# Kernel tuning notes

Hardware: AMD Instinct MI355X
Metric: run time of the kernel (lower is better)

The kernel has to match this reference:

```python
import jax, jax.numpy as jnp
import numpy as np

M, L, O, D, B = 512, 16, 32, 64, 16
GAMMA = 1.0 / (2.0 * D)  # RBF bandwidth ~ median sq-dist of randn data


def _rbf(X, Y):
    """Gaussian RBF kernel. X:[M,D]; Y:[M2,D] -> [M,M2] or Y:[B,L,D] -> [B,M,L]."""
    x2 = jnp.sum(X * X, axis=-1)
    y2 = jnp.sum(Y * Y, axis=-1)
    if Y.ndim == 3:
        d2 = x2[None, :, None] + y2[:, None, :] - 2.0 * jnp.einsum('md,bld->bml', X, Y)
    else:
        d2 = x2[:, None] + y2[None, :] - 2.0 * X @ Y.T
    return jnp.exp(-GAMMA * d2)


def setup_inputs() -> dict:
    key = jax.random.key(0)
    k1, k2, k3, k4 = jax.random.split(key, 4)
    inps = jax.random.normal(k1, (B, L, D), dtype=jnp.float32)
    nys_X = jax.random.normal(k2, (M, D), dtype=jnp.float32)
    nys_Y = jax.random.normal(k3, (M, D), dtype=jnp.float32)
    # xavier_uniform for (M*L, M*L)
    lim = float(np.sqrt(6.0 / (2 * M * L)))
    koopman = jax.random.uniform(k4, (M * L, M * L), dtype=jnp.float32, minval=-lim, maxval=lim)
    return {"inps": inps, "nys_X": nys_X, "nys_Y": nys_Y, "koopman": koopman}


def reference(inps, nys_X, nys_Y, koopman):
    scale = M ** (-0.5)
    KX = _rbf(nys_X, inps) * scale   # [B, M, L]
    KY = _rbf(nys_Y, nys_Y) * scale  # [M, M]
    out0 = KX.reshape(B, M * L)      # [B, M*L]

    def step(carry, _):
        nxt = carry @ koopman.T      # einsum('ij,bj->bi', G, out)
        return nxt, nxt

    _, outs = jax.lax.scan(step, out0, None, length=O)   # [O, B, M*L]
    outs = jnp.transpose(outs, (1, 2, 0)).reshape(B, M, L, O)
    outs = jnp.einsum('ij,bjlo->bilo', KY, outs)          # [B, M, L, O]
    outs = jnp.einsum('ja,bjlo->bloa', nys_Y, outs)       # [B, L, O, D]
    return outs
```

## Files before the change

kernel.cpp:

```cpp
#include <hip/hip_runtime.h>
#include <hip/hip_bf16.h>

#define M_  512
#define L_  16
#define O_  32
#define D_  64
#define B_  16
#define ML  8192
#define SLOT (B_*ML)

typedef __attribute__((ext_vector_type(8))) short short8;
typedef __attribute__((ext_vector_type(4))) float f32x4;

static constexpr float GAMMA = 1.0f / 128.0f;
static constexpr float SCALE = 0.0441941738241592f;

__device__ __forceinline__ float sqdiff4(const float4& x, const float4& y) {
    float dx = x.x - y.x, dy = x.y - y.y, dz = x.z - y.z, dw = x.w - y.w;
    return dx*dx + dy*dy + dz*dz + dw*dw;
}

__device__ __forceinline__ unsigned short f2bf(float x) {
    unsigned u = __float_as_uint(x);
    u = (u + 0x7FFFu + ((u >> 16) & 1u)) >> 16;
    return (unsigned short)u;
}

__global__ __launch_bounds__(256) void k_cast(const float* __restrict__ G,
                                              unsigned short* __restrict__ Gb) {
    size_t t = (size_t)blockIdx.x * 256 + threadIdx.x;
    const float4* p = (const float4*)(G + t * 8);
    float4 a = p[0], b = p[1];
    union { short8 v; unsigned short u[8]; } o;
    o.u[0] = f2bf(a.x); o.u[1] = f2bf(a.y); o.u[2] = f2bf(a.z); o.u[3] = f2bf(a.w);
    o.u[4] = f2bf(b.x); o.u[5] = f2bf(b.y); o.u[6] = f2bf(b.z); o.u[7] = f2bf(b.w);
    *(short8*)(Gb + t * 8) = o.v;
}

__global__ __launch_bounds__(256) void k_out0_dual(const float* __restrict__ inps,
                                                   const float* __restrict__ X,
                                                   float* __restrict__ S0,
                                                   unsigned short* __restrict__ C0) {
    int idx = blockIdx.x * 256 + threadIdx.x;
    int l = idx & (L_ - 1);
    int m = (idx >> 4) & (M_ - 1);
    int b = idx >> 13;
    const float* xr = X + m * D_;
    const float* yr = inps + (b * L_ + l) * D_;
    float d2 = 0.f;
#pragma unroll
    for (int d = 0; d < D_; d += 4) {
        float4 xv = *(const float4*)(xr + d);
        float4 yv = *(const float4*)(yr + d);
        d2 += sqdiff4(xv, yv);
    }
    float v = SCALE * expf(-GAMMA * d2);
    S0[idx] = v;
    C0[idx] = f2bf(v);
}

__global__ __launch_bounds__(256) void k_out0(const float* __restrict__ inps,
                                              const float* __restrict__ X,
                                              float* __restrict__ out0) {
    int idx = blockIdx.x * 256 + threadIdx.x;
    int l = idx & (L_ - 1);
    int m = (idx >> 4) & (M_ - 1);
    int b = idx >> 13;
    const float* xr = X + m * D_;
    const float* yr = inps + (b * L_ + l) * D_;
    float d2 = 0.f;
#pragma unroll
    for (int d = 0; d < D_; d += 4) {
        float4 xv = *(const float4*)(xr + d);
        float4 yv = *(const float4*)(yr + d);
        d2 += sqdiff4(xv, yv);
    }
    out0[idx] = SCALE * expf(-GAMMA * d2);
}

__global__ __launch_bounds__(256) void k_ky(const float* __restrict__ Y,
                                            float* __restrict__ KY) {
    int idx = blockIdx.x * 256 + threadIdx.x;
    int j = idx & (M_ - 1);
    int i = idx >> 9;
    const float* yi = Y + i * D_;
    const float* yj = Y + j * D_;
    float d2 = 0.f;
#pragma unroll
    for (int d = 0; d < D_; d += 4) {
        float4 a = *(const float4*)(yi + d);
        float4 b = *(const float4*)(yj + d);
        d2 += sqdiff4(a, b);
    }
    KY[idx] = SCALE * expf(-GAMMA * d2);
}

__global__ __launch_bounds__(256) void k_w(const float* __restrict__ KY,
                                           const float* __restrict__ Y,
                                           float* __restrict__ W) {
    int idx = blockIdx.x * 256 + threadIdx.x;
    int a = idx & (D_ - 1);
    int m = idx >> 6;
    float acc = 0.f;
    for (int j = 0; j < M_; ++j)
        acc = fmaf(KY[m * M_ + j], Y[j * D_ + a], acc);
    W[idx] = acc;
}

__global__ __launch_bounds__(512) void k_step_fused(const unsigned short* __restrict__ Gb,
                                                    const unsigned short* __restrict__ Cin,
                                                    float* __restrict__ Sout,
                                                    unsigned short* __restrict__ Cout) {
    const int i0   = blockIdx.x << 5;
    const int w    = threadIdx.x >> 6;
    const int lane = threadIdx.x & 63;
    const int r    = lane & 15;
    const int koff = (lane >> 4) << 3;
    const size_t kbase = (size_t)w * 1024 + koff;

    const unsigned short* a0 = Gb + (size_t)(i0 + r)      * ML + kbase;
    const unsigned short* a1 = Gb + (size_t)(i0 + 16 + r) * ML + kbase;
    const unsigned short* bp = Cin + (size_t)r * ML + kbase;

    f32x4 acc0 = {0.f, 0.f, 0.f, 0.f};
    f32x4 acc1 = {0.f, 0.f, 0.f, 0.f};
#pragma unroll 4
    for (int k = 0; k < 1024; k += 32) {
        short8 bv = *(const short8*)(bp + k);
        short8 av0 = *(const short8*)(a0 + k);
        short8 av1 = *(const short8*)(a1 + k);
        acc0 = __builtin_amdgcn_mfma_f32_16x16x32_bf16(av0, bv, acc0, 0, 0, 0);
        acc1 = __builtin_amdgcn_mfma_f32_16x16x32_bf16(av1, bv, acc1, 0, 0, 0);
    }

    __shared__ float red[8][512];
    const int rbase = (lane >> 4) << 2;
#pragma unroll
    for (int q = 0; q < 4; ++q) {
        red[w][(rbase + q) * 16 + r]       = acc0[q];
        red[w][256 + (rbase + q) * 16 + r] = acc1[q];
    }
    __syncthreads();

    const int tid = threadIdx.x;
    float s = red[0][tid] + red[1][tid] + red[2][tid] + red[3][tid] +
              red[4][tid] + red[5][tid] + red[6][tid] + red[7][tid];
    const int b = tid & 15;
    const int i = i0 + (tid >> 4);
    Sout[(size_t)b * ML + i] = s;
    Cout[(size_t)b * ML + i] = f2bf(s);
}

__global__ __launch_bounds__(256) void k_step(const float* __restrict__ G,
                                              const float* __restrict__ carry,
                                              float* __restrict__ out) {
    const int i = blockIdx.x;
    const float* __restrict__ grow = G + (size_t)i * ML;
    float acc[B_];
#pragma unroll
    for (int b = 0; b < B_; ++b) acc[b] = 0.f;
    for (int j0 = threadIdx.x * 4; j0 < ML; j0 += 256 * 4) {
        float4 g = *(const float4*)(grow + j0);
#pragma unroll
        for (int b = 0; b < B_; ++b) {
            float4 c = *(const float4*)(carry + b * ML + j0);
            acc[b] = fmaf(g.x, c.x, fmaf(g.y, c.y, fmaf(g.z, c.z, fmaf(g.w, c.w, acc[b]))));
        }
    }
#pragma unroll
    for (int b = 0; b < B_; ++b) {
        float v = acc[b];
#pragma unroll
        for (int off = 32; off > 0; off >>= 1) v += __shfl_down(v, off, 64);
        acc[b] = v;
    }
    __shared__ float red2[4][B_];
    int lane = threadIdx.x & 63;
    int wv   = threadIdx.x >> 6;
    if (lane == 0) {
#pragma unroll
        for (int b = 0; b < B_; ++b) red2[wv][b] = acc[b];
    }
    __syncthreads();
    if (threadIdx.x < B_) {
        float v = red2[0][threadIdx.x] + red2[1][threadIdx.x] +
                  red2[2][threadIdx.x] + red2[3][threadIdx.x];
        out[threadIdx.x * ML + i] = v;
    }
}

__global__ __launch_bounds__(256) void k_final(const float* __restrict__ S,
                                               const float* __restrict__ W,
                                               float* __restrict__ out) {
    int t = blockIdx.x * 256 + threadIdx.x;
    int a = t & (D_ - 1);
    int w = t >> 6;
    int o = w & (O_ - 1);
    int bl = w >> 5;
    int l = bl & (L_ - 1);
    int b = bl >> 4;
    const float* slot = S + (size_t)(o + 1) * SLOT + b * ML;
    float acc = 0.f;
    for (int m = 0; m < M_; ++m)
        acc = fmaf(slot[m * L_ + l], W[m * D_ + a], acc);
    out[t] = acc;
}

extern "C" void kernel_launch(void* const* d_in, const int* in_sizes, int n_in,
                              void* d_out, int out_size, void* d_ws, size_t ws_size,
                              hipStream_t stream) {
    const float* inps    = (const float*)d_in[0];
    const float* nys_X   = (const float*)d_in[1];
    const float* nys_Y   = (const float*)d_in[2];
    const float* koopman = (const float*)d_in[3];
    float* out = (float*)d_out;

    const size_t GB_BYTES  = (size_t)ML * ML * 2;
    const size_t S_BYTES   = (size_t)33 * SLOT * 4;
    const size_t CB_BYTES  = (size_t)33 * SLOT * 2;
    const size_t KY_BYTES  = (size_t)M_ * M_ * 4;
    const size_t W_BYTES   = (size_t)M_ * D_ * 4;
    const size_t NEED_FAST = GB_BYTES + S_BYTES + CB_BYTES + KY_BYTES + W_BYTES;

    if (ws_size >= NEED_FAST) {
        unsigned short* Gb = (unsigned short*)d_ws;
        float*          S  = (float*)((char*)d_ws + GB_BYTES);
        unsigned short* Cb = (unsigned short*)((char*)S + S_BYTES);
        float*          KY = (float*)((char*)Cb + CB_BYTES);
        float*          W  = KY + M_ * M_;

        k_cast<<<(int)((size_t)ML * ML / 8 / 256), 256, 0, stream>>>(koopman, Gb);
        k_out0_dual<<<SLOT / 256, 256, 0, stream>>>(inps, nys_X, S, Cb);
        k_ky<<<(M_ * M_) / 256, 256, 0, stream>>>(nys_Y, KY);
        k_w<<<(M_ * D_) / 256, 256, 0, stream>>>(KY, nys_Y, W);

        for (int o = 1; o <= O_; ++o) {
            k_step_fused<<<256, 512, 0, stream>>>(Gb,
                                                  Cb + (size_t)(o - 1) * SLOT,
                                                  S + (size_t)o * SLOT,
                                                  Cb + (size_t)o * SLOT);
        }
        k_final<<<(B_ * L_ * O_ * D_) / 256, 256, 0, stream>>>(S, W, out);
    } else {
        float* S  = (float*)d_ws;
        float* KY = S + (size_t)33 * SLOT;
        float* W  = KY + M_ * M_;

        k_out0<<<SLOT / 256, 256, 0, stream>>>(inps, nys_X, S);
        k_ky<<<(M_ * M_) / 256, 256, 0, stream>>>(nys_Y, KY);
        k_w<<<(M_ * D_) / 256, 256, 0, stream>>>(KY, nys_Y, W);
        for (int o = 1; o <= O_; ++o)
            k_step<<<ML, 256, 0, stream>>>(koopman, S + (size_t)(o - 1) * SLOT,
                                           S + (size_t)o * SLOT);
        k_final<<<(B_ * L_ * O_ * D_) / 256, 256, 0, stream>>>(S, W, out);
    }
}
```

Before: 958.7 us.

## Pre-pack Koopman matrix into MFMA fragment order and split rows over more blocks

The bf16 cast kernel now writes the Koopman matrix in a tile-packed layout, so each wave's A-fragment loads are fully contiguous 1 KB chunks instead of strided row reads. The step kernel now launches 512 blocks of 1024 threads, one 16-row tile per block, with 16 waves each reducing a 512-wide K slice through shared memory. This raises parallelism and coalescing for the bandwidth-bound 32 GEMV-like steps. In exchange the shared-memory reduction is larger, only a quarter of the threads take part in it, and the B fragment is now loaded once per A tile rather than reused across two tiles.

```diff
diff --git a/kernel.cpp b/kernel.cpp
--- a/kernel.cpp
+++ b/kernel.cpp
@@ -26,15 +26,21 @@
     return (unsigned short)u;
 }
 
-__global__ __launch_bounds__(256) void k_cast(const float* __restrict__ G,
-                                              unsigned short* __restrict__ Gb) {
-    size_t t = (size_t)blockIdx.x * 256 + threadIdx.x;
-    const float4* p = (const float4*)(G + t * 8);
-    float4 a = p[0], b = p[1];
+__global__ __launch_bounds__(256) void k_cast_pack(const float* __restrict__ G,
+                                                   unsigned short* __restrict__ Gp) {
+    int wid  = (blockIdx.x << 2) + (threadIdx.x >> 6);
+    int l    = threadIdx.x & 63;
+    int mt = wid >> 8;
+    int ks = wid & 255;
+    int r  = l & 15;
+    int kk = l >> 4;
+    const float* src = G + (size_t)(mt * 16 + r) * ML + ks * 32 + kk * 8;
+    float4 a = *(const float4*)(src);
+    float4 b = *(const float4*)(src + 4);
     union { short8 v; unsigned short u[8]; } o;
     o.u[0] = f2bf(a.x); o.u[1] = f2bf(a.y); o.u[2] = f2bf(a.z); o.u[3] = f2bf(a.w);
     o.u[4] = f2bf(b.x); o.u[5] = f2bf(b.y); o.u[6] = f2bf(b.z); o.u[7] = f2bf(b.w);
-    *(short8*)(Gb + t * 8) = o.v;
+    *(short8*)(Gp + ((size_t)(mt * 256 + ks) * 64 + l) * 8) = o.v;
 }
 
 __global__ __launch_bounds__(256) void k_out0_dual(const float* __restrict__ inps,
@@ -107,48 +113,44 @@
     W[idx] = acc;
 }
 
-__global__ __launch_bounds__(512) void k_step_fused(const unsigned short* __restrict__ Gb,
-                                                    const unsigned short* __restrict__ Cin,
-                                                    float* __restrict__ Sout,
-                                                    unsigned short* __restrict__ Cout) {
-    const int i0   = blockIdx.x << 5;
+__global__ __launch_bounds__(1024, 8) void k_step_packed(const unsigned short* __restrict__ Gp,
+                                                         const unsigned short* __restrict__ Cin,
+                                                         float* __restrict__ Sout,
+                                                         unsigned short* __restrict__ Cout) {
+    const int mt   = blockIdx.x;
     const int w    = threadIdx.x >> 6;
     const int lane = threadIdx.x & 63;
     const int r    = lane & 15;
-    const int koff = (lane >> 4) << 3;
-    const size_t kbase = (size_t)w * 1024 + koff;
-
-    const unsigned short* a0 = Gb + (size_t)(i0 + r)      * ML + kbase;
-    const unsigned short* a1 = Gb + (size_t)(i0 + 16 + r) * ML + kbase;
-    const unsigned short* bp = Cin + (size_t)r * ML + kbase;
-
-    f32x4 acc0 = {0.f, 0.f, 0.f, 0.f};
-    f32x4 acc1 = {0.f, 0.f, 0.f, 0.f};
+    const int kk   = lane >> 4;
+
+    const unsigned short* ap = Gp + ((size_t)(mt * 256 + w * 16) * 64 + lane) * 8;
+    const unsigned short* bp = Cin + (size_t)r * ML + w * 512 + kk * 8;
+
+    f32x4 acc = {0.f, 0.f, 0.f, 0.f};
 #pragma unroll 4
-    for (int k = 0; k < 1024; k += 32) {
-        short8 bv = *(const short8*)(bp + k);
-        short8 av0 = *(const short8*)(a0 + k);
-        short8 av1 = *(const short8*)(a1 + k);
-        acc0 = __builtin_amdgcn_mfma_f32_16x16x32_bf16(av0, bv, acc0, 0, 0, 0);
-        acc1 = __builtin_amdgcn_mfma_f32_16x16x32_bf16(av1, bv, acc1, 0, 0, 0);
-    }
-
-    __shared__ float red[8][512];
-    const int rbase = (lane >> 4) << 2;
-#pragma unroll
-    for (int q = 0; q < 4; ++q) {
-        red[w][(rbase + q) * 16 + r]       = acc0[q];
-        red[w][256 + (rbase + q) * 16 + r] = acc1[q];
-    }
+    for (int it = 0; it < 16; ++it) {
+        short8 a = *(const short8*)(ap + (size_t)it * 512);
+        short8 b = *(const short8*)(bp + it * 32);
+        acc = __builtin_amdgcn_mfma_f32_16x16x32_bf16(a, b, acc, 0, 0, 0);
+    }
+
+    __shared__ float red[16][256];
+    const int rbase = kk << 2;
+#pragma unroll
+    for (int q = 0; q < 4; ++q)
+        red[w][(rbase + q) * 16 + r] = acc[q];
     __syncthreads();
 
     const int tid = threadIdx.x;
-    float s = red[0][tid] + red[1][tid] + red[2][tid] + red[3][tid] +
-              red[4][tid] + red[5][tid] + red[6][tid] + red[7][tid];
-    const int b = tid & 15;
-    const int i = i0 + (tid >> 4);
-    Sout[(size_t)b * ML + i] = s;
-    Cout[(size_t)b * ML + i] = f2bf(s);
+    if (tid < 256) {
+        float s = 0.f;
+#pragma unroll
+        for (int p = 0; p < 16; ++p) s += red[p][tid];
+        const int b = tid & 15;
+        const int i = (mt << 4) + (tid >> 4);
+        Sout[(size_t)b * ML + i] = s;
+        Cout[(size_t)b * ML + i] = f2bf(s);
+    }
 }
 
 __global__ __launch_bounds__(256) void k_step(const float* __restrict__ G,
@@ -223,22 +225,22 @@
     const size_t NEED_FAST = GB_BYTES + S_BYTES + CB_BYTES + KY_BYTES + W_BYTES;
 
     if (ws_size >= NEED_FAST) {
-        unsigned short* Gb = (unsigned short*)d_ws;
+        unsigned short* Gp = (unsigned short*)d_ws;
         float*          S  = (float*)((char*)d_ws + GB_BYTES);
         unsigned short* Cb = (unsigned short*)((char*)S + S_BYTES);
         float*          KY = (float*)((char*)Cb + CB_BYTES);
         float*          W  = KY + M_ * M_;
 
-        k_cast<<<(int)((size_t)ML * ML / 8 / 256), 256, 0, stream>>>(koopman, Gb);
+        k_cast_pack<<<32768, 256, 0, stream>>>(koopman, Gp);
         k_out0_dual<<<SLOT / 256, 256, 0, stream>>>(inps, nys_X, S, Cb);
         k_ky<<<(M_ * M_) / 256, 256, 0, stream>>>(nys_Y, KY);
         k_w<<<(M_ * D_) / 256, 256, 0, stream>>>(KY, nys_Y, W);
 
         for (int o = 1; o <= O_; ++o) {
-            k_step_fused<<<256, 512, 0, stream>>>(Gb,
-                                                  Cb + (size_t)(o - 1) * SLOT,
-                                                  S + (size_t)o * SLOT,
-                                                  Cb + (size_t)o * SLOT);
+            k_step_packed<<<512, 1024, 0, stream>>>(Gp,
+                                                    Cb + (size_t)(o - 1) * SLOT,
+                                                    S + (size_t)o * SLOT,
+                                                    Cb + (size_t)o * SLOT);
         }
         k_final<<<(B_ * L_ * O_ * D_) / 256, 256, 0, stream>>>(S, W, out);
     } else {
```

After: 992.4 us. +3.5%, slower.
